# Kernel optimization log

Measured on AMD Instinct MI355X. Metric: run time of the kernel, lower is better.

## Reference

```python
import jax, jax.numpy as jnp
import numpy as np

N_NODES = 100000
N_EDGES = 1600000
B_GRAPHS = 64
F_IN = 128
HID = 128
N_CLS = 16
EPS = 1e-5


def setup_inputs() -> dict:
    key = jax.random.key(0)
    ks = jax.random.split(key, 12)
    x = jax.random.normal(ks[0], (N_NODES, F_IN), jnp.float32)
    edge_index = jax.random.randint(ks[1], (2, N_EDGES), 0, N_NODES, dtype=jnp.int32)
    batch = jnp.sort(jax.random.randint(ks[2], (N_NODES,), 0, B_GRAPHS, dtype=jnp.int32))
    sc = lambda fi: 1.0 / np.sqrt(fi)
    return {
        'x': x, 'edge_index': edge_index, 'batch': batch,
        'W1': jax.random.normal(ks[3], (F_IN, HID), jnp.float32) * sc(F_IN),
        'b1': jnp.zeros((HID,), jnp.float32),
        'g1': jnp.ones((HID,), jnp.float32), 'be1': jnp.zeros((HID,), jnp.float32),
        'W2': jax.random.normal(ks[4], (HID, HID), jnp.float32) * sc(HID),
        'b2': jnp.zeros((HID,), jnp.float32),
        'g2': jnp.ones((HID,), jnp.float32), 'be2': jnp.zeros((HID,), jnp.float32),
        'Wg1': jax.random.normal(ks[5], (HID, HID // 2), jnp.float32) * sc(HID),
        'bg1': jnp.zeros((HID // 2,), jnp.float32),
        'Wg2': jax.random.normal(ks[6], (HID // 2, 1), jnp.float32) * sc(HID // 2),
        'bg2': jnp.zeros((1,), jnp.float32),
        'Wc': jax.random.normal(ks[7], (HID, N_CLS), jnp.float32) * sc(HID),
        'bc': jnp.zeros((N_CLS,), jnp.float32),
    }


def gcn_conv(x, src, dst, W, b):
    # GCNConv: h = D^{-1/2}(A+I)D^{-1/2} (x W) + b, self-loops added
    n = x.shape[0]
    h = x @ W
    loop = jnp.arange(n, dtype=src.dtype)
    s = jnp.concatenate([src, loop])
    d = jnp.concatenate([dst, loop])
    deg = jax.ops.segment_sum(jnp.ones_like(d, dtype=h.dtype), d, num_segments=n)
    dinv = jax.lax.rsqrt(deg)  # deg >= 1 thanks to self-loops
    norm = dinv[s] * dinv[d]           # [E+N]
    msg = h[s] * norm[:, None]         # [E+N, HID] gather-transform
    return jax.ops.segment_sum(msg, d, num_segments=n) + b  # scatter-add


def layernorm(x, g, be):
    mu = jnp.mean(x, axis=-1, keepdims=True)
    var = jnp.mean(jnp.square(x - mu), axis=-1, keepdims=True)
    return (x - mu) * jax.lax.rsqrt(var + EPS) * g + be


def att_pool(x, batch, Wg1, bg1, Wg2, bg2, n_graphs):
    gate = jax.nn.relu(x @ Wg1 + bg1) @ Wg2 + bg2           # [N,1]
    gmax = jax.ops.segment_max(gate, batch, num_segments=n_graphs)
    e = jnp.exp(gate - gmax[batch])
    denom = jax.ops.segment_sum(e, batch, num_segments=n_graphs)
    alpha = e / denom[batch]                                 # segment softmax
    return jax.ops.segment_sum(alpha * x, batch, num_segments=n_graphs)


def reference(x, edge_index, batch, W1, b1, g1, be1, W2, b2, g2, be2,
              Wg1, bg1, Wg2, bg2, Wc, bc):
    src, dst = edge_index[0], edge_index[1]
    h = gcn_conv(x, src, dst, W1, b1)
    h = jax.nn.relu(layernorm(h, g1, be1))  # dropout is identity at eval
    h = gcn_conv(h, src, dst, W2, b2)
    h = jax.nn.relu(layernorm(h, g2, be2))
    pooled = att_pool(h, batch, Wg1, bg1, Wg2, bg2, B_GRAPHS)  # [B, HID]
    return pooled @ Wc + bc  # [B, N_CLS]
```

## Files before the change

kernel.cpp:

```cpp
#include <hip/hip_runtime.h>


typedef unsigned short ushort_t;
typedef unsigned int uint_t;
typedef __attribute__((ext_vector_type(8))) short short8;
typedef __attribute__((ext_vector_type(4))) float floatx4;

#define POOL_S 16
#define PAD_DEG 64
#define BW_SH 7
#define BUCKET_W 128
#define NBMAX 1024
#define CAP 4096
#define CHUNK 4096

__device__ inline ushort_t bf16_rn(float f) {
  uint_t u = __float_as_uint(f);
  u += 0x7fffu + ((u >> 16) & 1u);
  return (ushort_t)(u >> 16);
}
__device__ inline float bf16_lo(uint_t v) { return __uint_as_float(v << 16); }
__device__ inline float bf16_hi(uint_t v) { return __uint_as_float(v & 0xffff0000u); }
__device__ inline uint_t bf16_pack(float a, float b) {
  return (uint_t)bf16_rn(a) | ((uint_t)bf16_rn(b) << 16);
}

__global__ __launch_bounds__(256) void init_kernel(
    int* __restrict__ gcount, const float* __restrict__ W1,
    const float* __restrict__ W2, const float* __restrict__ Wg1,
    ushort_t* __restrict__ Wt, uint_t* __restrict__ hs_rowN) {
  int id = blockIdx.x * 256 + threadIdx.x;
  if (id < NBMAX) { gcount[id] = 0; return; }
  int id2 = id - NBMAX;
  if (id2 < 40960) {
    float v;
    if (id2 < 16384) {
      int n = id2 >> 7, k = id2 & 127;
      v = W1[k * 128 + n];
    } else if (id2 < 32768) {
      int i2 = id2 - 16384;
      int n = i2 >> 7, k = i2 & 127;
      v = W2[k * 128 + n];
    } else {
      int i2 = id2 - 32768;
      int n = i2 >> 7, k = i2 & 127;
      v = Wg1[k * 64 + n];
    }
    Wt[id2] = bf16_rn(v);
    return;
  }
  int id3 = id2 - 40960;
  if (id3 < 64) hs_rowN[id3] = 0;
}

template <int TM, int NC, bool IN_F32, bool SCALE, bool BIASRELU, bool GATEDOT>
__device__ __forceinline__ void gemm_tile(
    const void* __restrict__ in, const ushort_t* __restrict__ Wt,
    const float* __restrict__ bias, const float* __restrict__ dinv,
    ushort_t* __restrict__ out, int M, int row0,
    const float* __restrict__ Wg2, const float* __restrict__ bg2,
    float* __restrict__ gate_out, short* As) {
  constexpr int CT = NC / 16;
  constexpr int RT = TM / 64;
  const int t = threadIdx.x;
#pragma unroll
  for (int i = 0; i < TM / 16; ++i) {
    int chunk = t + i * 256;
    int rr = chunk >> 4, c8 = (chunk & 15) * 8;
    int row = row0 + rr;
    short8 val = {0, 0, 0, 0, 0, 0, 0, 0};
    if (IN_F32) {
      const float* inf = (const float*)in;
      if (row < M) {
        float4 v0 = *(const float4*)(inf + (size_t)row * 128 + c8);
        float4 v1 = *(const float4*)(inf + (size_t)row * 128 + c8 + 4);
        val[0] = (short)bf16_rn(v0.x); val[1] = (short)bf16_rn(v0.y);
        val[2] = (short)bf16_rn(v0.z); val[3] = (short)bf16_rn(v0.w);
        val[4] = (short)bf16_rn(v1.x); val[5] = (short)bf16_rn(v1.y);
        val[6] = (short)bf16_rn(v1.z); val[7] = (short)bf16_rn(v1.w);
      }
    } else {
      const short* inb = (const short*)in;
      if (row < M) val = *(const short8*)(inb + (size_t)row * 128 + c8);
    }
    *(short8*)&As[rr * 136 + c8] = val;
  }
  __syncthreads();

  const int wave = t >> 6, lane = t & 63;
  const int m16 = lane & 15, quad = lane >> 4;
  floatx4 acc[RT][CT];
#pragma unroll
  for (int rt = 0; rt < RT; ++rt)
#pragma unroll
    for (int ct = 0; ct < CT; ++ct) acc[rt][ct] = (floatx4){0.f, 0.f, 0.f, 0.f};
#pragma unroll
  for (int ks = 0; ks < 4; ++ks) {
    int koff = ks * 32 + quad * 8;
    short8 a[RT];
#pragma unroll
    for (int rt = 0; rt < RT; ++rt)
      a[rt] = *(const short8*)&As[(wave * 16 + rt * 64 + m16) * 136 + koff];
#pragma unroll
    for (int ct = 0; ct < CT; ++ct) {
      short8 b = *(const short8*)((const short*)Wt + (size_t)(ct * 16 + m16) * 128 + koff);
#pragma unroll
      for (int rt = 0; rt < RT; ++rt)
        acc[rt][ct] = __builtin_amdgcn_mfma_f32_16x16x32_bf16(a[rt], b, acc[rt][ct], 0, 0, 0);
    }
  }

  float bv[CT];
  if (BIASRELU) {
#pragma unroll
    for (int ct = 0; ct < CT; ++ct) bv[ct] = bias[ct * 16 + m16];
  }

  if (GATEDOT) {
    float w2[CT];
#pragma unroll
    for (int ct = 0; ct < CT; ++ct) w2[ct] = Wg2[ct * 16 + m16];
    float bg2v = bg2[0];
#pragma unroll
    for (int rt = 0; rt < RT; ++rt) {
#pragma unroll
      for (int reg = 0; reg < 4; ++reg) {
        float p = 0.f;
#pragma unroll
        for (int ct = 0; ct < CT; ++ct)
          p += fmaxf(acc[rt][ct][reg] + bv[ct], 0.f) * w2[ct];
        p += __shfl_xor(p, 1);
        p += __shfl_xor(p, 2);
        p += __shfl_xor(p, 4);
        p += __shfl_xor(p, 8);
        if (m16 == 0) {
          int row = row0 + wave * 16 + rt * 64 + quad * 4 + reg;
          if (row < M) gate_out[row] = p + bg2v;
        }
      }
    }
    return;
  }

#pragma unroll
  for (int rt = 0; rt < RT; ++rt) {
#pragma unroll
    for (int reg = 0; reg < 4; ++reg) {
      int row = row0 + wave * 16 + rt * 64 + quad * 4 + reg;
      if (row < M) {
        float mult = SCALE ? dinv[row] : 1.f;
#pragma unroll
        for (int ct = 0; ct < CT; ++ct) {
          float v = acc[rt][ct][reg];
          if (BIASRELU) v = fmaxf(v + bv[ct], 0.f);
          else if (SCALE) v *= mult;
          out[(size_t)row * NC + ct * 16 + m16] = bf16_rn(v);
        }
      }
    }
  }
}

__global__ __launch_bounds__(256) void bin_gemm1_kernel(
    const int* __restrict__ src, const int* __restrict__ dst,
    int* __restrict__ gcount, int* __restrict__ buckets, int E,
    const float* __restrict__ x, const ushort_t* __restrict__ Wt,
    ushort_t* __restrict__ hs, int M, int nBin, int nGemm) {
  __shared__ __align__(16) char smem[64 * 136 * 2];
  short* As = (short*)smem;
  int* cntL = (int*)smem;
  int* offL = (int*)(smem + 4096);
  int b = blockIdx.x;
  int gi = b >> 1;
  if (b & 1) {
    if (gi < nGemm)
      gemm_tile<64, 128, true, false, false, false>(
          x, Wt, nullptr, nullptr, hs, M, gi * 64, nullptr, nullptr, nullptr, As);
    return;
  }
  if (gi < nBin) {
    const int t = threadIdx.x;
    const int base = gi * CHUNK;
    int c = E - base;
    if (c > CHUNK) c = CHUNK;
    const int cv = c & ~3;
    for (int i = t; i < NBMAX; i += 256) cntL[i] = 0;
    __syncthreads();
    for (int i = t * 4; i + 3 < c; i += 1024) {
      int4 d4 = *(const int4*)(dst + base + i);
      atomicAdd(&cntL[d4.x >> BW_SH], 1);
      atomicAdd(&cntL[d4.y >> BW_SH], 1);
      atomicAdd(&cntL[d4.z >> BW_SH], 1);
      atomicAdd(&cntL[d4.w >> BW_SH], 1);
    }
    for (int i = cv + t; i < c; i += 256)
      atomicAdd(&cntL[dst[base + i] >> BW_SH], 1);
    __syncthreads();
    for (int i = t; i < NBMAX; i += 256) {
      int cn = cntL[i];
      offL[i] = cn ? atomicAdd(&gcount[i], cn) : 0;
    }
    __syncthreads();
    for (int i = t * 4; i + 3 < c; i += 1024) {
      int4 d4 = *(const int4*)(dst + base + i);
      int4 s4 = *(const int4*)(src + base + i);
      int bk0 = d4.x >> BW_SH, bk1 = d4.y >> BW_SH;
      int bk2 = d4.z >> BW_SH, bk3 = d4.w >> BW_SH;
      int p0 = atomicAdd(&offL[bk0], 1);
      int p1 = atomicAdd(&offL[bk1], 1);
      int p2 = atomicAdd(&offL[bk2], 1);
      int p3 = atomicAdd(&offL[bk3], 1);
      if (p0 < CAP)
        buckets[(size_t)bk0 * CAP + p0] = (s4.x << BW_SH) | (d4.x & (BUCKET_W - 1));
      if (p1 < CAP)
        buckets[(size_t)bk1 * CAP + p1] = (s4.y << BW_SH) | (d4.y & (BUCKET_W - 1));
      if (p2 < CAP)
        buckets[(size_t)bk2 * CAP + p2] = (s4.z << BW_SH) | (d4.z & (BUCKET_W - 1));
      if (p3 < CAP)
        buckets[(size_t)bk3 * CAP + p3] = (s4.w << BW_SH) | (d4.w & (BUCKET_W - 1));
    }
    for (int i = cv + t; i < c; i += 256) {
      int s = src[base + i];
      int d = dst[base + i];
      int bk = d >> BW_SH;
      int pos = atomicAdd(&offL[bk], 1);
      if (pos < CAP)
        buckets[(size_t)bk * CAP + pos] = (s << BW_SH) | (d & (BUCKET_W - 1));
    }
  }
}

__global__ __launch_bounds__(256) void build_kernel(
    const int* __restrict__ gcount, const int* __restrict__ buckets,
    int* __restrict__ fill, int* __restrict__ srcs_pad, int N) {
  __shared__ int fillL[BUCKET_W];
  __shared__ alignas(16) int srcsL[BUCKET_W * PAD_DEG];
  const int b = blockIdx.x, t = threadIdx.x;
  if (t < BUCKET_W) fillL[t] = 0;
  __syncthreads();
  int cnt = gcount[b];
  if (cnt > CAP) cnt = CAP;
  const int cv = cnt & ~3;
  const int* bk = buckets + (size_t)b * CAP;
  for (int i = t * 4; i + 3 < cnt; i += 1024) {
    int4 v4 = *(const int4*)(bk + i);
#pragma unroll
    for (int j = 0; j < 4; ++j) {
      int v = (j == 0) ? v4.x : (j == 1) ? v4.y : (j == 2) ? v4.z : v4.w;
      int local = v & (BUCKET_W - 1);
      int s = (int)(((uint_t)v) >> BW_SH);
      int p = atomicAdd(&fillL[local], 1);
      if (p < PAD_DEG) srcsL[local * PAD_DEG + p] = s;
    }
  }
  for (int i = cv + t; i < cnt; i += 256) {
    int v = bk[i];
    int local = v & (BUCKET_W - 1);
    int s = (int)(((uint_t)v) >> BW_SH);
    int p = atomicAdd(&fillL[local], 1);
    if (p < PAD_DEG) srcsL[local * PAD_DEG + p] = s;
  }
  __syncthreads();
  const int node0 = b << BW_SH;
  int width = N - node0;
  if (width <= 0) return;
  if (width > BUCKET_W) width = BUCKET_W;
  if (t < width) fill[node0 + t] = fillL[t];
  const int tot4 = (width * PAD_DEG) >> 2;
  int4* dstp = (int4*)(srcs_pad + (size_t)node0 * PAD_DEG);
  const int4* srcp = (const int4*)srcsL;
  for (int j = t; j < tot4; j += 256) dstp[j] = srcp[j];
}

template <int NC, bool SCALE, bool BIASRELU, bool GATEDOT>
__global__ __launch_bounds__(256) void gemm_mfma_kernel(
    const ushort_t* __restrict__ in, const ushort_t* __restrict__ Wt,
    const float* __restrict__ bias, const float* __restrict__ dinv,
    ushort_t* __restrict__ out, int M,
    const float* __restrict__ Wg2, const float* __restrict__ bg2,
    float* __restrict__ gate_out) {
  __shared__ short As[128 * 136];
  gemm_tile<128, NC, false, SCALE, BIASRELU, GATEDOT>(
      in, Wt, bias, dinv, out, M, blockIdx.x * 128, Wg2, bg2, gate_out, As);
}

__device__ __forceinline__ void fma8(float* a, uint4 v, float e) {
  a[0] = fmaf(bf16_lo(v.x), e, a[0]); a[1] = fmaf(bf16_hi(v.x), e, a[1]);
  a[2] = fmaf(bf16_lo(v.y), e, a[2]); a[3] = fmaf(bf16_hi(v.y), e, a[3]);
  a[4] = fmaf(bf16_lo(v.z), e, a[4]); a[5] = fmaf(bf16_hi(v.z), e, a[5]);
  a[6] = fmaf(bf16_lo(v.w), e, a[6]); a[7] = fmaf(bf16_hi(v.w), e, a[7]);
}

template <bool PERSRC>
__global__ __launch_bounds__(256) void aggregate_ln_kernel(
    const ushort_t* __restrict__ hs, const int* __restrict__ fill,
    const int* __restrict__ srcs_pad, float* __restrict__ dinv,
    const float* __restrict__ bias, const float* __restrict__ gamma,
    const float* __restrict__ beta, ushort_t* __restrict__ out, int N) {
  int n = (blockIdx.x * 256 + threadIdx.x) >> 6;
  int lane = threadIdx.x & 63;
  if (n >= N) return;
  const int col = lane & 15, epar = lane >> 4;
  const uint4* hs4 = (const uint4*)hs;
  int sreg = srcs_pad[(size_t)n * PAD_DEG + lane];
  int count = fill[n];
  if (count > PAD_DEG) count = PAD_DEG;
  const int K = (count + 3) & ~3;
  float dv = rsqrtf((float)(count + 1));
  int sc = N;
  float dreg = 0.f;
  if (lane < count) {
    sc = sreg;
    if (PERSRC) dreg = rsqrtf((float)(fill[sc] + 1));
    else        dreg = 1.f;
  }
  float a[8] = {0.f, 0.f, 0.f, 0.f, 0.f, 0.f, 0.f, 0.f};
  int i = epar;
  for (; i + 12 < K; i += 16) {
    int s0 = __shfl(sc, i);       float e0 = __shfl(dreg, i);
    int s1 = __shfl(sc, i + 4);   float e1 = __shfl(dreg, i + 4);
    int s2 = __shfl(sc, i + 8);   float e2 = __shfl(dreg, i + 8);
    int s3 = __shfl(sc, i + 12);  float e3 = __shfl(dreg, i + 12);
    uint4 v0 = hs4[(size_t)s0 * 16 + col];
    uint4 v1 = hs4[(size_t)s1 * 16 + col];
    uint4 v2 = hs4[(size_t)s2 * 16 + col];
    uint4 v3 = hs4[(size_t)s3 * 16 + col];
    fma8(a, v0, e0); fma8(a, v1, e1); fma8(a, v2, e2); fma8(a, v3, e3);
  }
  for (; i < K; i += 4) {
    int s = __shfl(sc, i);
    float e = __shfl(dreg, i);
    uint4 v = hs4[(size_t)s * 16 + col];
    fma8(a, v, e);
  }
#pragma unroll
  for (int k = 0; k < 8; ++k) {
    a[k] += __shfl_xor(a[k], 16);
    a[k] += __shfl_xor(a[k], 32);
  }
  {
    uint4 sv = hs4[(size_t)n * 16 + col];
    fma8(a, sv, PERSRC ? dv : 1.f);
  }
  if (PERSRC && lane == 0) dinv[n] = dv;
  float4 b0 = *(const float4*)(bias + 8 * col);
  float4 b1 = *(const float4*)(bias + 8 * col + 4);
  float y[8];
  y[0] = a[0] * dv + b0.x; y[1] = a[1] * dv + b0.y;
  y[2] = a[2] * dv + b0.z; y[3] = a[3] * dv + b0.w;
  y[4] = a[4] * dv + b1.x; y[5] = a[5] * dv + b1.y;
  y[6] = a[6] * dv + b1.z; y[7] = a[7] * dv + b1.w;
  float s1 = 0.f, s2 = 0.f;
#pragma unroll
  for (int k = 0; k < 8; ++k) { s1 += y[k]; s2 += y[k] * y[k]; }
#pragma unroll
  for (int off = 1; off <= 8; off <<= 1) {
    s1 += __shfl_xor(s1, off);
    s2 += __shfl_xor(s2, off);
  }
  float mu = s1 * (1.f / 128.f);
  float var = s2 * (1.f / 128.f) - mu * mu;
  float rinv = rsqrtf(var + 1e-5f);
  float4 g0 = *(const float4*)(gamma + 8 * col);
  float4 g1 = *(const float4*)(gamma + 8 * col + 4);
  float4 e0 = *(const float4*)(beta + 8 * col);
  float4 e1 = *(const float4*)(beta + 8 * col + 4);
  float o[8];
  o[0] = fmaxf((y[0] - mu) * rinv * g0.x + e0.x, 0.f);
  o[1] = fmaxf((y[1] - mu) * rinv * g0.y + e0.y, 0.f);
  o[2] = fmaxf((y[2] - mu) * rinv * g0.z + e0.z, 0.f);
  o[3] = fmaxf((y[3] - mu) * rinv * g0.w + e0.w, 0.f);
  o[4] = fmaxf((y[4] - mu) * rinv * g1.x + e1.x, 0.f);
  o[5] = fmaxf((y[5] - mu) * rinv * g1.y + e1.y, 0.f);
  o[6] = fmaxf((y[6] - mu) * rinv * g1.z + e1.z, 0.f);
  o[7] = fmaxf((y[7] - mu) * rinv * g1.w + e1.w, 0.f);
  if (epar == 0) {
    uint4 pk;
    pk.x = bf16_pack(o[0], o[1]); pk.y = bf16_pack(o[2], o[3]);
    pk.z = bf16_pack(o[4], o[5]); pk.w = bf16_pack(o[6], o[7]);
    ((uint4*)out)[(size_t)n * 16 + col] = pk;
  }
}

__device__ inline int lower_bound_i(const int* a, int n, int key) {
  int lo = 0, hi = n;
  while (lo < hi) {
    int mid = (lo + hi) >> 1;
    if (a[mid] < key) lo = mid + 1; else hi = mid;
  }
  return lo;
}

__global__ __launch_bounds__(256) void pool_partial_kernel(
    const ushort_t* __restrict__ h2, const float* __restrict__ gate,
    const int* __restrict__ batch, float* __restrict__ partial,
    float2* __restrict__ pstat, int N) {
  int g = blockIdx.x / POOL_S, sub = blockIdx.x % POOL_S;
  int t = threadIdx.x;
  __shared__ float redx[256];
  __shared__ float redy[256];
  __shared__ float s_m;
  int lo = lower_bound_i(batch, N, g);
  int hi = lower_bound_i(batch, N, g + 1);
  int len = hi - lo;
  int chunk = (len + POOL_S - 1) / POOL_S;
  int a = lo + sub * chunk;
  int b = a + chunk < hi ? a + chunk : hi;
  float m = -3.4e38f;
  for (int i = a + t; i < b; i += 256) m = fmaxf(m, gate[i]);
  redx[t] = m;
  __syncthreads();
  for (int off = 128; off; off >>= 1) {
    if (t < off) redx[t] = fmaxf(redx[t], redx[t + off]);
    __syncthreads();
  }
  if (t == 0) s_m = redx[0];
  __syncthreads();
  float gmax = s_m;
  __syncthreads();
  float ssum = 0.f;
  for (int i = a + t; i < b; i += 256) ssum += expf(gate[i] - gmax);
  redx[t] = ssum;
  __syncthreads();
  for (int off = 128; off; off >>= 1) {
    if (t < off) redx[t] += redx[t + off];
    __syncthreads();
  }
  float denom = redx[0];
  __syncthreads();
  int p = t & 63, strm = t >> 6;
  const uint_t* h2u = (const uint_t*)h2;
  float accx = 0.f, accy = 0.f;
  int i = a + strm;
  for (; i + 8 <= b; i += 8) {
    float e0 = expf(gate[i] - gmax);
    float e1 = expf(gate[i + 4] - gmax);
    uint_t v0 = h2u[(size_t)i * 64 + p];
    uint_t v1 = h2u[(size_t)(i + 4) * 64 + p];
    accx += e0 * bf16_lo(v0) + e1 * bf16_lo(v1);
    accy += e0 * bf16_hi(v0) + e1 * bf16_hi(v1);
  }
  for (; i < b; i += 4) {
    float e = expf(gate[i] - gmax);
    uint_t v = h2u[(size_t)i * 64 + p];
    accx += e * bf16_lo(v);
    accy += e * bf16_hi(v);
  }
  redx[t] = accx;
  redy[t] = accy;
  __syncthreads();
  if (t < 64) {
    float px = redx[t] + redx[t + 64] + redx[t + 128] + redx[t + 192];
    float py = redy[t] + redy[t + 64] + redy[t + 128] + redy[t + 192];
    float* dstp = partial + (size_t)blockIdx.x * 128;
    dstp[2 * t] = px;
    dstp[2 * t + 1] = py;
  }
  if (t == 0) pstat[blockIdx.x] = make_float2(gmax, denom);
}

__global__ __launch_bounds__(128) void classify_kernel(
    const float* __restrict__ partial, const float2* __restrict__ pstat,
    const float* __restrict__ Wc, const float* __restrict__ bc,
    float* __restrict__ out) {
  int g = blockIdx.x, t = threadIdx.x;
  __shared__ float pooled[128];
  __shared__ float wgt[POOL_S];
  __shared__ float s_inv;
  if (t == 0) {
    float M = -3.4e38f;
    float2 st[POOL_S];
#pragma unroll
    for (int k = 0; k < POOL_S; ++k) {
      st[k] = pstat[g * POOL_S + k];
      M = fmaxf(M, st[k].x);
    }
    float total = 0.f;
#pragma unroll
    for (int k = 0; k < POOL_S; ++k) {
      float w = expf(st[k].x - M);
      wgt[k] = w;
      total += st[k].y * w;
    }
    s_inv = total > 0.f ? 1.f / total : 0.f;
  }
  __syncthreads();
  float inv = s_inv;
  float s = 0.f;
#pragma unroll
  for (int k = 0; k < POOL_S; ++k)
    s += partial[((size_t)g * POOL_S + k) * 128 + t] * wgt[k];
  pooled[t] = s * inv;
  __syncthreads();
  if (t < 16) {
    float o = bc[t];
    for (int ff = 0; ff < 128; ++ff) o = fmaf(pooled[ff], Wc[ff * 16 + t], o);
    out[g * 16 + t] = o;
  }
}

extern "C" void kernel_launch(void* const* d_in, const int* in_sizes, int n_in,
                              void* d_out, int out_size, void* d_ws, size_t ws_size,
                              hipStream_t stream) {
  const float* x   = (const float*)d_in[0];
  const int*   ei  = (const int*)d_in[1];
  const int*   bat = (const int*)d_in[2];
  const float* W1  = (const float*)d_in[3];
  const float* b1  = (const float*)d_in[4];
  const float* g1  = (const float*)d_in[5];
  const float* be1 = (const float*)d_in[6];
  const float* W2  = (const float*)d_in[7];
  const float* b2  = (const float*)d_in[8];
  const float* g2  = (const float*)d_in[9];
  const float* be2 = (const float*)d_in[10];
  const float* Wg1 = (const float*)d_in[11];
  const float* bg1 = (const float*)d_in[12];
  const float* Wg2 = (const float*)d_in[13];
  const float* bg2 = (const float*)d_in[14];
  const float* Wc  = (const float*)d_in[15];
  const float* bc  = (const float*)d_in[16];

  const int N = in_sizes[0] / 128;
  const int E = in_sizes[1] / 2;
  const int B = out_size / 16;
  const int* src = ei;
  const int* dst = ei + E;

  const int Np = (N + 3) & ~3;

  int* fill      = (int*)d_ws;
  float* dinv    = (float*)(fill + Np);
  float* gatep   = dinv + Np;
  int* gcount    = (int*)(gatep + Np);
  float2* pstat  = (float2*)(gcount + NBMAX);
  float* ppart   = (float*)(pstat + B * POOL_S);
  int* srcs_pad  = (int*)(ppart + (size_t)B * POOL_S * 128);
  ushort_t* Wt   = (ushort_t*)(srcs_pad + (size_t)N * PAD_DEG);
  ushort_t* hs   = Wt + 40960;
  ushort_t* h1   = hs + (size_t)128 * (N + 1);
  int* buckets   = (int*)h1;

  const int NB = (N + BUCKET_W - 1) >> BW_SH;
  const int nBin = (E + CHUNK - 1) / CHUNK;
  const int Gb64 = (N + 63) / 64;
  const int Gg128 = (N + 127) / 128;

  int initIds = NBMAX + 40960 + 64;
  init_kernel<<<(initIds + 255) / 256, 256, 0, stream>>>(
      gcount, W1, W2, Wg1, Wt, (uint_t*)(hs + (size_t)128 * N));

  int nPairs = nBin > Gb64 ? nBin : Gb64;
  bin_gemm1_kernel<<<2 * nPairs, 256, 0, stream>>>(
      src, dst, gcount, buckets, E, x, Wt, hs, N, nBin, Gb64);

  build_kernel<<<NB, 256, 0, stream>>>(gcount, buckets, fill, srcs_pad, N);

  aggregate_ln_kernel<true><<<(N + 3) / 4, 256, 0, stream>>>(
      hs, fill, srcs_pad, dinv, b1, g1, be1, h1, N);
  gemm_mfma_kernel<128, true, false, false><<<Gg128, 256, 0, stream>>>(
      h1, Wt + 16384, nullptr, dinv, hs, N, nullptr, nullptr, nullptr);
  aggregate_ln_kernel<false><<<(N + 3) / 4, 256, 0, stream>>>(
      hs, fill, srcs_pad, dinv, b2, g2, be2, h1, N);
  gemm_mfma_kernel<64, false, true, true><<<Gg128, 256, 0, stream>>>(
      h1, Wt + 32768, bg1, nullptr, nullptr, N, Wg2, bg2, gatep);

  pool_partial_kernel<<<B * POOL_S, 256, 0, stream>>>(
      h1, gatep, bat, ppart, pstat, N);
  classify_kernel<<<B, 128, 0, stream>>>(ppart, pstat, Wc, bc, (float*)d_out);
}
```

Measured before the change: 383.4 us.

## Sort edge chunk by bucket in shared memory before coalesced bucket writes

The binning blocks now run a local counting sort of each 4096-edge chunk in LDS: they histogram the buckets, take a block-wide prefix scan, and scatter the packed edges into a shared sorted array. Each wave then copies contiguous per-bucket runs to the global bucket arrays. Before, every edge was a random 4-byte global store, and this change is meant to turn those into mostly contiguous stores. The cost is extra LDS traffic, a 256-step scan with many barriers, and a larger shared-memory footprint, which may lower occupancy.

```diff
diff --git a/kernel.cpp b/kernel.cpp
--- a/kernel.cpp
+++ b/kernel.cpp
@@ -166,67 +166,103 @@
     int* __restrict__ gcount, int* __restrict__ buckets, int E,
     const float* __restrict__ x, const ushort_t* __restrict__ Wt,
     ushort_t* __restrict__ hs, int M, int nBin, int nGemm) {
-  __shared__ __align__(16) char smem[64 * 136 * 2];
-  short* As = (short*)smem;
-  int* cntL = (int*)smem;
-  int* offL = (int*)(smem + 4096);
+  __shared__ __align__(16) char smem[28688];
   int b = blockIdx.x;
   int gi = b >> 1;
   if (b & 1) {
     if (gi < nGemm)
       gemm_tile<64, 128, true, false, false, false>(
-          x, Wt, nullptr, nullptr, hs, M, gi * 64, nullptr, nullptr, nullptr, As);
+          x, Wt, nullptr, nullptr, hs, M, gi * 64, nullptr, nullptr, nullptr,
+          (short*)smem);
     return;
   }
-  if (gi < nBin) {
-    const int t = threadIdx.x;
-    const int base = gi * CHUNK;
-    int c = E - base;
-    if (c > CHUNK) c = CHUNK;
-    const int cv = c & ~3;
-    for (int i = t; i < NBMAX; i += 256) cntL[i] = 0;
+  if (gi >= nBin) return;
+  int* sortedL = (int*)smem;
+  int* startL  = (int*)(smem + 16384);
+  int* curL    = (int*)(smem + 20496);
+  int* ogL     = (int*)(smem + 24592);
+  int* scanL   = sortedL;
+
+  const int t = threadIdx.x;
+  const int base = gi * CHUNK;
+  int c = E - base;
+  if (c > CHUNK) c = CHUNK;
+  const int cv = c & ~3;
+
+  for (int i = t; i < NBMAX; i += 256) curL[i] = 0;
+  __syncthreads();
+  for (int i = t * 4; i + 3 < c; i += 1024) {
+    int4 d4 = *(const int4*)(dst + base + i);
+    atomicAdd(&curL[d4.x >> BW_SH], 1);
+    atomicAdd(&curL[d4.y >> BW_SH], 1);
+    atomicAdd(&curL[d4.z >> BW_SH], 1);
+    atomicAdd(&curL[d4.w >> BW_SH], 1);
+  }
+  for (int i = cv + t; i < c; i += 256)
+    atomicAdd(&curL[dst[base + i] >> BW_SH], 1);
+  __syncthreads();
+
+  const int b0 = 4 * t;
+  int c0 = curL[b0], c1 = curL[b0 + 1], c2 = curL[b0 + 2], c3 = curL[b0 + 3];
+  int tsum = c0 + c1 + c2 + c3;
+  scanL[t] = tsum;
+  __syncthreads();
+  for (int off = 1; off < 256; off <<= 1) {
+    int add = (t >= off) ? scanL[t - off] : 0;
     __syncthreads();
-    for (int i = t * 4; i + 3 < c; i += 1024) {
-      int4 d4 = *(const int4*)(dst + base + i);
-      atomicAdd(&cntL[d4.x >> BW_SH], 1);
-      atomicAdd(&cntL[d4.y >> BW_SH], 1);
-      atomicAdd(&cntL[d4.z >> BW_SH], 1);
-      atomicAdd(&cntL[d4.w >> BW_SH], 1);
-    }
-    for (int i = cv + t; i < c; i += 256)
-      atomicAdd(&cntL[dst[base + i] >> BW_SH], 1);
+    scanL[t] += add;
     __syncthreads();
-    for (int i = t; i < NBMAX; i += 256) {
-      int cn = cntL[i];
-      offL[i] = cn ? atomicAdd(&gcount[i], cn) : 0;
-    }
-    __syncthreads();
-    for (int i = t * 4; i + 3 < c; i += 1024) {
-      int4 d4 = *(const int4*)(dst + base + i);
-      int4 s4 = *(const int4*)(src + base + i);
-      int bk0 = d4.x >> BW_SH, bk1 = d4.y >> BW_SH;
-      int bk2 = d4.z >> BW_SH, bk3 = d4.w >> BW_SH;
-      int p0 = atomicAdd(&offL[bk0], 1);
-      int p1 = atomicAdd(&offL[bk1], 1);
-      int p2 = atomicAdd(&offL[bk2], 1);
-      int p3 = atomicAdd(&offL[bk3], 1);
-      if (p0 < CAP)
-        buckets[(size_t)bk0 * CAP + p0] = (s4.x << BW_SH) | (d4.x & (BUCKET_W - 1));
-      if (p1 < CAP)
-        buckets[(size_t)bk1 * CAP + p1] = (s4.y << BW_SH) | (d4.y & (BUCKET_W - 1));
-      if (p2 < CAP)
-        buckets[(size_t)bk2 * CAP + p2] = (s4.z << BW_SH) | (d4.z & (BUCKET_W - 1));
-      if (p3 < CAP)
-        buckets[(size_t)bk3 * CAP + p3] = (s4.w << BW_SH) | (d4.w & (BUCKET_W - 1));
-    }
-    for (int i = cv + t; i < c; i += 256) {
-      int s = src[base + i];
-      int d = dst[base + i];
-      int bk = d >> BW_SH;
-      int pos = atomicAdd(&offL[bk], 1);
-      if (pos < CAP)
-        buckets[(size_t)bk * CAP + pos] = (s << BW_SH) | (d & (BUCKET_W - 1));
-    }
+  }
+  int tincl = scanL[t];
+  __syncthreads();
+  int tbase = tincl - tsum;
+
+  startL[b0]     = tbase;
+  startL[b0 + 1] = tbase + c0;
+  startL[b0 + 2] = tbase + c0 + c1;
+  startL[b0 + 3] = tbase + c0 + c1 + c2;
+  if (t == 255) startL[NBMAX] = tincl;
+  ogL[b0]     = c0 ? atomicAdd(&gcount[b0], c0) : 0;
+  ogL[b0 + 1] = c1 ? atomicAdd(&gcount[b0 + 1], c1) : 0;
+  ogL[b0 + 2] = c2 ? atomicAdd(&gcount[b0 + 2], c2) : 0;
+  ogL[b0 + 3] = c3 ? atomicAdd(&gcount[b0 + 3], c3) : 0;
+  curL[b0]     = tbase;
+  curL[b0 + 1] = tbase + c0;
+  curL[b0 + 2] = tbase + c0 + c1;
+  curL[b0 + 3] = tbase + c0 + c1 + c2;
+  __syncthreads();
+
+  for (int i = t * 4; i + 3 < c; i += 1024) {
+    int4 d4 = *(const int4*)(dst + base + i);
+    int4 s4 = *(const int4*)(src + base + i);
+    int bk, p;
+    bk = d4.x >> BW_SH; p = atomicAdd(&curL[bk], 1);
+    sortedL[p] = (s4.x << BW_SH) | (d4.x & (BUCKET_W - 1));
+    bk = d4.y >> BW_SH; p = atomicAdd(&curL[bk], 1);
+    sortedL[p] = (s4.y << BW_SH) | (d4.y & (BUCKET_W - 1));
+    bk = d4.z >> BW_SH; p = atomicAdd(&curL[bk], 1);
+    sortedL[p] = (s4.z << BW_SH) | (d4.z & (BUCKET_W - 1));
+    bk = d4.w >> BW_SH; p = atomicAdd(&curL[bk], 1);
+    sortedL[p] = (s4.w << BW_SH) | (d4.w & (BUCKET_W - 1));
+  }
+  for (int i = cv + t; i < c; i += 256) {
+    int s = src[base + i];
+    int d = dst[base + i];
+    int bk = d >> BW_SH;
+    int p = atomicAdd(&curL[bk], 1);
+    sortedL[p] = (s << BW_SH) | (d & (BUCKET_W - 1));
+  }
+  __syncthreads();
+
+  const int wave = t >> 6, lane = t & 63;
+  for (int bk = wave; bk < NBMAX; bk += 4) {
+    int st = startL[bk];
+    int cn = startL[bk + 1] - st;
+    if (cn == 0) continue;
+    int og = ogL[bk];
+    size_t gb = (size_t)bk * CAP + og;
+    for (int j = lane; j < cn; j += 64)
+      if (og + j < CAP) buckets[gb + j] = sortedL[st + j];
   }
 }
 
```

After: 394.3 us. 1.03x slower.

## Fuse gate MLP into second aggregation and merge pooling with classifier

Applied to the files above, without the earlier changes.

Computes the attention-gate MLP (Wg1 then ReLU then Wg2) per node inside the second aggregate+LayerNorm kernel, using a swizzled shared-memory copy of Wg1 and scalar FMAs. This removes the separate gate GEMM launch and its reread of h2. The partial pooling and classifier are merged into one kernel, where the last block per graph, found with an atomic counter, does the final reduction. The binning chunk size is also doubled. In exchange, every aggregation block reloads 16KB of Wg1 into shared memory and adds scalar FMA work that previously ran on MFMA.

```diff
diff --git a/kernel.cpp b/kernel.cpp
--- a/kernel.cpp
+++ b/kernel.cpp
@@ -12,7 +12,7 @@
 #define BUCKET_W 128
 #define NBMAX 1024
 #define CAP 4096
-#define CHUNK 4096
+#define CHUNK 8192
 
 __device__ inline ushort_t bf16_rn(float f) {
   uint_t u = __float_as_uint(f);
@@ -21,6 +21,9 @@
 }
 __device__ inline float bf16_lo(uint_t v) { return __uint_as_float(v << 16); }
 __device__ inline float bf16_hi(uint_t v) { return __uint_as_float(v & 0xffff0000u); }
+__device__ inline float bf16_s(short s) {
+  return __uint_as_float(((uint_t)(ushort_t)s) << 16);
+}
 __device__ inline uint_t bf16_pack(float a, float b) {
   return (uint_t)bf16_rn(a) | ((uint_t)bf16_rn(b) << 16);
 }
@@ -28,7 +31,8 @@
 __global__ __launch_bounds__(256) void init_kernel(
     int* __restrict__ gcount, const float* __restrict__ W1,
     const float* __restrict__ W2, const float* __restrict__ Wg1,
-    ushort_t* __restrict__ Wt, uint_t* __restrict__ hs_rowN) {
+    ushort_t* __restrict__ Wt, uint_t* __restrict__ hs_rowN,
+    int* __restrict__ doneCnt, int B) {
   int id = blockIdx.x * 256 + threadIdx.x;
   if (id < NBMAX) { gcount[id] = 0; return; }
   int id2 = id - NBMAX;
@@ -50,16 +54,16 @@
     return;
   }
   int id3 = id2 - 40960;
-  if (id3 < 64) hs_rowN[id3] = 0;
-}
-
-template <int TM, int NC, bool IN_F32, bool SCALE, bool BIASRELU, bool GATEDOT>
+  if (id3 < 64) { hs_rowN[id3] = 0; return; }
+  int id4 = id3 - 64;
+  if (id4 < B) doneCnt[id4] = 0;
+}
+
+template <int TM, int NC, bool IN_F32, bool SCALE>
 __device__ __forceinline__ void gemm_tile(
     const void* __restrict__ in, const ushort_t* __restrict__ Wt,
-    const float* __restrict__ bias, const float* __restrict__ dinv,
-    ushort_t* __restrict__ out, int M, int row0,
-    const float* __restrict__ Wg2, const float* __restrict__ bg2,
-    float* __restrict__ gate_out, short* As) {
+    const float* __restrict__ dinv, ushort_t* __restrict__ out,
+    int M, int row0, short* As) {
   constexpr int CT = NC / 16;
   constexpr int RT = TM / 64;
   const int t = threadIdx.x;
@@ -110,38 +114,6 @@
     }
   }
 
-  float bv[CT];
-  if (BIASRELU) {
-#pragma unroll
-    for (int ct = 0; ct < CT; ++ct) bv[ct] = bias[ct * 16 + m16];
-  }
-
-  if (GATEDOT) {
-    float w2[CT];
-#pragma unroll
-    for (int ct = 0; ct < CT; ++ct) w2[ct] = Wg2[ct * 16 + m16];
-    float bg2v = bg2[0];
-#pragma unroll
-    for (int rt = 0; rt < RT; ++rt) {
-#pragma unroll
-      for (int reg = 0; reg < 4; ++reg) {
-        float p = 0.f;
-#pragma unroll
-        for (int ct = 0; ct < CT; ++ct)
-          p += fmaxf(acc[rt][ct][reg] + bv[ct], 0.f) * w2[ct];
-        p += __shfl_xor(p, 1);
-        p += __shfl_xor(p, 2);
-        p += __shfl_xor(p, 4);
-        p += __shfl_xor(p, 8);
-        if (m16 == 0) {
-          int row = row0 + wave * 16 + rt * 64 + quad * 4 + reg;
-          if (row < M) gate_out[row] = p + bg2v;
-        }
-      }
-    }
-    return;
-  }
-
 #pragma unroll
   for (int rt = 0; rt < RT; ++rt) {
 #pragma unroll
@@ -152,8 +124,7 @@
 #pragma unroll
         for (int ct = 0; ct < CT; ++ct) {
           float v = acc[rt][ct][reg];
-          if (BIASRELU) v = fmaxf(v + bv[ct], 0.f);
-          else if (SCALE) v *= mult;
+          if (SCALE) v *= mult;
           out[(size_t)row * NC + ct * 16 + m16] = bf16_rn(v);
         }
       }
@@ -174,8 +145,7 @@
   int gi = b >> 1;
   if (b & 1) {
     if (gi < nGemm)
-      gemm_tile<64, 128, true, false, false, false>(
-          x, Wt, nullptr, nullptr, hs, M, gi * 64, nullptr, nullptr, nullptr, As);
+      gemm_tile<64, 128, true, false>(x, Wt, nullptr, hs, M, gi * 64, As);
     return;
   }
   if (gi < nBin) {
@@ -272,16 +242,12 @@
   for (int j = t; j < tot4; j += 256) dstp[j] = srcp[j];
 }
 
-template <int NC, bool SCALE, bool BIASRELU, bool GATEDOT>
+template <int NC, bool SCALE>
 __global__ __launch_bounds__(256) void gemm_mfma_kernel(
     const ushort_t* __restrict__ in, const ushort_t* __restrict__ Wt,
-    const float* __restrict__ bias, const float* __restrict__ dinv,
-    ushort_t* __restrict__ out, int M,
-    const float* __restrict__ Wg2, const float* __restrict__ bg2,
-    float* __restrict__ gate_out) {
+    const float* __restrict__ dinv, ushort_t* __restrict__ out, int M) {
   __shared__ short As[128 * 136];
-  gemm_tile<128, NC, false, SCALE, BIASRELU, GATEDOT>(
-      in, Wt, bias, dinv, out, M, blockIdx.x * 128, Wg2, bg2, gate_out, As);
+  gemm_tile<128, NC, false, SCALE>(in, Wt, dinv, out, M, blockIdx.x * 128, As);
 }
 
 __device__ __forceinline__ void fma8(float* a, uint4 v, float e) {
@@ -291,14 +257,30 @@
   a[6] = fmaf(bf16_lo(v.w), e, a[6]); a[7] = fmaf(bf16_hi(v.w), e, a[7]);
 }
 
-template <bool PERSRC>
+template <bool PERSRC, bool GATE>
 __global__ __launch_bounds__(256) void aggregate_ln_kernel(
     const ushort_t* __restrict__ hs, const int* __restrict__ fill,
     const int* __restrict__ srcs_pad, float* __restrict__ dinv,
     const float* __restrict__ bias, const float* __restrict__ gamma,
-    const float* __restrict__ beta, ushort_t* __restrict__ out, int N) {
-  int n = (blockIdx.x * 256 + threadIdx.x) >> 6;
-  int lane = threadIdx.x & 63;
+    const float* __restrict__ beta, ushort_t* __restrict__ out, int N,
+    const ushort_t* __restrict__ Wg1t, const float* __restrict__ Wg2,
+    const float* __restrict__ bg1, const float* __restrict__ bg2,
+    float* __restrict__ gate_out) {
+  extern __shared__ char dynsmem[];
+  short* Wg1L = (short*)dynsmem;
+  uint4* h2L  = (uint4*)(dynsmem + 16384);
+  const int tt = threadIdx.x;
+  if (GATE) {
+#pragma unroll
+    for (int i = tt; i < 1024; i += 256) {
+      int row = i >> 4, c8i = i & 15;
+      *(short8*)&Wg1L[row * 128 + 8 * (c8i ^ (row & 7))] =
+          *(const short8*)(Wg1t + row * 128 + c8i * 8);
+    }
+    __syncthreads();
+  }
+  int n = (blockIdx.x * 256 + tt) >> 6;
+  int lane = tt & 63;
   if (n >= N) return;
   const int col = lane & 15, epar = lane >> 4;
   const uint4* hs4 = (const uint4*)hs;
@@ -374,11 +356,38 @@
   o[5] = fmaxf((y[5] - mu) * rinv * g1.y + e1.y, 0.f);
   o[6] = fmaxf((y[6] - mu) * rinv * g1.z + e1.z, 0.f);
   o[7] = fmaxf((y[7] - mu) * rinv * g1.w + e1.w, 0.f);
+  uint4 pk;
+  pk.x = bf16_pack(o[0], o[1]); pk.y = bf16_pack(o[2], o[3]);
+  pk.z = bf16_pack(o[4], o[5]); pk.w = bf16_pack(o[6], o[7]);
+  const int wv = tt >> 6;
   if (epar == 0) {
-    uint4 pk;
-    pk.x = bf16_pack(o[0], o[1]); pk.y = bf16_pack(o[2], o[3]);
-    pk.z = bf16_pack(o[4], o[5]); pk.w = bf16_pack(o[6], o[7]);
     ((uint4*)out)[(size_t)n * 16 + col] = pk;
+    if (GATE) h2L[wv * 16 + col] = pk;
+  }
+  if (GATE) {
+    __threadfence_block();
+    float accg = bg1[lane];
+#pragma unroll
+    for (int f8 = 0; f8 < 16; ++f8) {
+      uint4 hv = h2L[wv * 16 + f8];
+      short8 w8 = *(const short8*)&Wg1L[lane * 128 + 8 * (f8 ^ (lane & 7))];
+      accg = fmaf(bf16_lo(hv.x), bf16_s(w8[0]), accg);
+      accg = fmaf(bf16_hi(hv.x), bf16_s(w8[1]), accg);
+      accg = fmaf(bf16_lo(hv.y), bf16_s(w8[2]), accg);
+      accg = fmaf(bf16_hi(hv.y), bf16_s(w8[3]), accg);
+      accg = fmaf(bf16_lo(hv.z), bf16_s(w8[4]), accg);
+      accg = fmaf(bf16_hi(hv.z), bf16_s(w8[5]), accg);
+      accg = fmaf(bf16_lo(hv.w), bf16_s(w8[6]), accg);
+      accg = fmaf(bf16_hi(hv.w), bf16_s(w8[7]), accg);
+    }
+    float p = fmaxf(accg, 0.f) * Wg2[lane];
+    p += __shfl_xor(p, 1);
+    p += __shfl_xor(p, 2);
+    p += __shfl_xor(p, 4);
+    p += __shfl_xor(p, 8);
+    p += __shfl_xor(p, 16);
+    p += __shfl_xor(p, 32);
+    if (lane == 0) gate_out[n] = p + bg2[0];
   }
 }
 
@@ -391,15 +400,20 @@
   return lo;
 }
 
-__global__ __launch_bounds__(256) void pool_partial_kernel(
+__global__ __launch_bounds__(256) void pool_classify_kernel(
     const ushort_t* __restrict__ h2, const float* __restrict__ gate,
     const int* __restrict__ batch, float* __restrict__ partial,
-    float2* __restrict__ pstat, int N) {
+    float2* __restrict__ pstat, int N, const float* __restrict__ Wc,
+    const float* __restrict__ bc, float* __restrict__ out,
+    int* __restrict__ doneCnt) {
   int g = blockIdx.x / POOL_S, sub = blockIdx.x % POOL_S;
   int t = threadIdx.x;
   __shared__ float redx[256];
   __shared__ float redy[256];
   __shared__ float s_m;
+  __shared__ int s_last;
+  __shared__ float wgtL[POOL_S];
+  __shared__ float s_inv;
   int lo = lower_bound_i(batch, N, g);
   int hi = lower_bound_i(batch, N, g + 1);
   int len = hi - lo;
@@ -457,16 +471,12 @@
     dstp[2 * t + 1] = py;
   }
   if (t == 0) pstat[blockIdx.x] = make_float2(gmax, denom);
-}
-
-__global__ __launch_bounds__(128) void classify_kernel(
-    const float* __restrict__ partial, const float2* __restrict__ pstat,
-    const float* __restrict__ Wc, const float* __restrict__ bc,
-    float* __restrict__ out) {
-  int g = blockIdx.x, t = threadIdx.x;
-  __shared__ float pooled[128];
-  __shared__ float wgt[POOL_S];
-  __shared__ float s_inv;
+  __syncthreads();
+  __threadfence();
+  if (t == 0) s_last = (atomicAdd(&doneCnt[g], 1) == POOL_S - 1);
+  __syncthreads();
+  if (!s_last) return;
+  __threadfence();
   if (t == 0) {
     float M = -3.4e38f;
     float2 st[POOL_S];
@@ -479,22 +489,24 @@
 #pragma unroll
     for (int k = 0; k < POOL_S; ++k) {
       float w = expf(st[k].x - M);
-      wgt[k] = w;
+      wgtL[k] = w;
       total += st[k].y * w;
     }
     s_inv = total > 0.f ? 1.f / total : 0.f;
   }
   __syncthreads();
   float inv = s_inv;
-  float s = 0.f;
-#pragma unroll
-  for (int k = 0; k < POOL_S; ++k)
-    s += partial[((size_t)g * POOL_S + k) * 128 + t] * wgt[k];
-  pooled[t] = s * inv;
+  if (t < 128) {
+    float s = 0.f;
+#pragma unroll
+    for (int k = 0; k < POOL_S; ++k)
+      s += partial[((size_t)g * POOL_S + k) * 128 + t] * wgtL[k];
+    redx[t] = s * inv;
+  }
   __syncthreads();
   if (t < 16) {
     float o = bc[t];
-    for (int ff = 0; ff < 128; ++ff) o = fmaf(pooled[ff], Wc[ff * 16 + t], o);
+    for (int ff = 0; ff < 128; ++ff) o = fmaf(redx[ff], Wc[ff * 16 + t], o);
     out[g * 16 + t] = o;
   }
 }
@@ -532,7 +544,8 @@
   float* dinv    = (float*)(fill + Np);
   float* gatep   = dinv + Np;
   int* gcount    = (int*)(gatep + Np);
-  float2* pstat  = (float2*)(gcount + NBMAX);
+  int* doneCnt   = gcount + NBMAX;
+  float2* pstat  = (float2*)(doneCnt + B);
   float* ppart   = (float*)(pstat + B * POOL_S);
   int* srcs_pad  = (int*)(ppart + (size_t)B * POOL_S * 128);
   ushort_t* Wt   = (ushort_t*)(srcs_pad + (size_t)N * PAD_DEG);
@@ -545,9 +558,9 @@
   const int Gb64 = (N + 63) / 64;
   const int Gg128 = (N + 127) / 128;
 
-  int initIds = NBMAX + 40960 + 64;
+  int initIds = NBMAX + 40960 + 64 + B;
   init_kernel<<<(initIds + 255) / 256, 256, 0, stream>>>(
-      gcount, W1, W2, Wg1, Wt, (uint_t*)(hs + (size_t)128 * N));
+      gcount, W1, W2, Wg1, Wt, (uint_t*)(hs + (size_t)128 * N), doneCnt, B);
 
   int nPairs = nBin > Gb64 ? nBin : Gb64;
   bin_gemm1_kernel<<<2 * nPairs, 256, 0, stream>>>(
@@ -555,16 +568,15 @@
 
   build_kernel<<<NB, 256, 0, stream>>>(gcount, buckets, fill, srcs_pad, N);
 
-  aggregate_ln_kernel<true><<<(N + 3) / 4, 256, 0, stream>>>(
-      hs, fill, srcs_pad, dinv, b1, g1, be1, h1, N);
-  gemm_mfma_kernel<128, true, false, false><<<Gg128, 256, 0, stream>>>(
-      h1, Wt + 16384, nullptr, dinv, hs, N, nullptr, nullptr, nullptr);
-  aggregate_ln_kernel<false><<<(N + 3) / 4, 256, 0, stream>>>(
-      hs, fill, srcs_pad, dinv, b2, g2, be2, h1, N);
-  gemm_mfma_kernel<64, false, true, true><<<Gg128, 256, 0, stream>>>(
-      h1, Wt + 32768, bg1, nullptr, nullptr, N, Wg2, bg2, gatep);
-
-  pool_partial_kernel<<<B * POOL_S, 256, 0, stream>>>(
-      h1, gatep, bat, ppart, pstat, N);
-  classify_kernel<<<B, 128, 0, stream>>>(ppart, pstat, Wc, bc, (float*)d_out);
-}
+  aggregate_ln_kernel<true, false><<<(N + 3) / 4, 256, 0, stream>>>(
+      hs, fill, srcs_pad, dinv, b1, g1, be1, h1, N,
+      nullptr, nullptr, nullptr, nullptr, nullptr);
+  gemm_mfma_kernel<128, true><<<Gg128, 256, 0, stream>>>(
+      h1, Wt + 16384, dinv, hs, N);
+  aggregate_ln_kernel<false, true><<<(N + 3) / 4, 256, 17408, stream>>>(
+      hs, fill, srcs_pad, dinv, b2, g2, be2, h1, N,
+      Wt + 32768, Wg2, bg1, bg2, gatep);
+
+  pool_classify_kernel<<<B * POOL_S, 256, 0, stream>>>(
+      h1, gatep, bat, ppart, pstat, N, Wc, bc, (float*)d_out, doneCnt);
+}
```

Result: slower. 495.5 us (+29.2%).
